# Optimization experiments

Measured on AMD Instinct MI355X. Metric: run time of the kernel, lower is better.

The kernel has to match this reference:

```python
import jax, jax.numpy as jnp
import numpy as np
from jax import lax

CLIP = 0.2
GAMMA = 1.0
LAM = 0.95
B, S = 256, 16384


def setup_inputs() -> dict:
    key = jax.random.key(0)
    k0, k1, k2, k3, k4, k5 = jax.random.split(key, 6)
    return {
        "rewards": jax.random.normal(k0, (B, S), jnp.float32),
        "values": jax.random.normal(k1, (B, S), jnp.float32),
        "new_log_probs": jax.random.normal(k2, (B, S), jnp.float32),
        "old_log_probs": jax.random.normal(k3, (B, S), jnp.float32),
        "new_values": jax.random.normal(k4, (B, S), jnp.float32),
        "act_masks": jax.random.randint(k5, (B, S), 0, 2, jnp.int32),
    }


def _mask_mean(loss, mask):
    # (loss * mask).sum(-1) / clamp(mask.sum(-1), 1e-8)
    return (loss * mask).sum(-1) / jnp.maximum(mask.sum(-1), 1e-8)


def _gae(rewards, values):
    # delta_t = r_t + gamma * V_{t+1} - V_t   (V_S := 0 bootstrap)
    next_values = jnp.concatenate([values[:, 1:], jnp.zeros_like(values[:, :1])], axis=1)
    deltas = rewards + GAMMA * next_values - values  # [B,S]
    decay = GAMMA * LAM

    def step(gae, delta):  # reverse-time linear recurrence
        gae = delta + decay * gae
        return gae, gae

    _, adv = lax.scan(step, jnp.zeros(deltas.shape[0], deltas.dtype), deltas.T, reverse=True)
    advantages = adv.T  # [B,S], in forward time order
    returns = advantages + values
    return advantages, returns


def reference(rewards, values, new_log_probs, old_log_probs, new_values, act_masks):
    mask = act_masks.astype(rewards.dtype)
    advantages, returns = _gae(rewards, values)

    # clipped PPO surrogate
    ratio = jnp.exp(new_log_probs - old_log_probs)
    surr1 = ratio * advantages
    surr2 = jnp.clip(ratio, 1.0 - CLIP, 1.0 + CLIP) * advantages
    p_loss = _mask_mean(-jnp.minimum(surr1, surr2), mask)  # [B]

    # masked value MSE against GAE returns
    v_loss = _mask_mean((new_values - returns) ** 2, mask)  # [B]

    return jnp.stack([p_loss, v_loss])  # [2, B]
```

## Files before the change

kernel.cpp:

```cpp
#include <hip/hip_runtime.h>

constexpr int B_DIM  = 256;
constexpr int S_DIM  = 16384;
constexpr int SEG    = 1024;
constexpr int NSEG   = S_DIM / SEG;
constexpr int HALO   = 256;
constexpr float DECAY   = 0.95f;
constexpr float CLIP_LO = 0.8f;
constexpr float CLIP_HI = 1.2f;

__host__ __device__ constexpr float fpow(float x, int n) {
    float r = 1.0f;
    for (int i = 0; i < n; ++i) r *= x;
    return r;
}

__device__ __forceinline__ float dpow4(int e) {
    float p = 1.0f;
    if (e & 1)  p *= fpow(DECAY, 4);
    if (e & 2)  p *= fpow(DECAY, 8);
    if (e & 4)  p *= fpow(DECAY, 16);
    if (e & 8)  p *= fpow(DECAY, 32);
    if (e & 16) p *= fpow(DECAY, 64);
    if (e & 32) p *= fpow(DECAY, 128);
    return p;
}

__global__ __launch_bounds__(256) void ppo_seg(
    const float* __restrict__ rewards,
    const float* __restrict__ values,
    const float* __restrict__ nlp,
    const float* __restrict__ olp,
    const float* __restrict__ nval,
    const int*   __restrict__ amask,
    double* __restrict__ part)
{
    const int l   = threadIdx.x & 63;
    const int wid = (blockIdx.x << 2) | (threadIdx.x >> 6);
    const int row = wid >> 4;
    const int seg = wid & 15;
    const size_t base = (size_t)row * S_DIM + (size_t)seg * SEG;
    const size_t i4   = base + 4 * (size_t)l;

    float4 r4[4], v4[4];
    #pragma unroll
    for (int q = 0; q < 4; ++q) {
        r4[q] = *reinterpret_cast<const float4*>(rewards + i4 + 256 * q);
        v4[q] = *reinterpret_cast<const float4*>(values  + i4 + 256 * q);
    }

    float G = 0.0f;
    float v_end = 0.0f;
    if (seg < NSEG - 1) {
        float4 rh = *reinterpret_cast<const float4*>(rewards + i4 + SEG);
        float4 vh = *reinterpret_cast<const float4*>(values  + i4 + SEG);
        float vhe = values[base + SEG + HALO];
        float vn = __shfl(vh.x, (l + 1) & 63);
        if (l == 63) vn = vhe;
        const float d0 = rh.x + vh.y - vh.x;
        const float d1 = rh.y + vh.z - vh.y;
        const float d2 = rh.z + vh.w - vh.z;
        const float d3 = rh.w + vn   - vh.w;
        const float c  = fmaf(DECAY, fmaf(DECAY, fmaf(DECAY, d3, d2), d1), d0);
        float u = dpow4(l) * c;
        #pragma unroll
        for (int m = 1; m < 64; m <<= 1) u += __shfl_xor(u, m);
        G = u;
        v_end = __shfl(vh.x, 0);
    }

    const float h1 = __shfl(v4[1].x, 0);
    const float h2 = __shfl(v4[2].x, 0);
    const float h3 = __shfl(v4[3].x, 0);
    const float nx[4] = {h1, h2, h3, v_end};

    float d[16];
    #pragma unroll
    for (int q = 0; q < 4; ++q) {
        float vn = __shfl(v4[q].x, (l + 1) & 63);
        if (l == 63) vn = nx[q];
        d[4*q+0] = r4[q].x + v4[q].y - v4[q].x;
        d[4*q+1] = r4[q].y + v4[q].z - v4[q].y;
        d[4*q+2] = r4[q].z + v4[q].w - v4[q].z;
        d[4*q+3] = r4[q].w + vn      - v4[q].w;
    }

    float s[4];
    #pragma unroll
    for (int q = 0; q < 4; ++q)
        s[q] = fmaf(DECAY, fmaf(DECAY, fmaf(DECAY, d[4*q+3], d[4*q+2]), d[4*q+1]), d[4*q+0]);

    #pragma unroll
    for (int st = 1; st < 64; st <<= 1) {
        const float f = fpow(DECAY, 4 * st);
        #pragma unroll
        for (int q = 0; q < 4; ++q) {
            float o = __shfl(s[q], min(l + st, 63));
            s[q] = (l < 64 - st) ? fmaf(f, o, s[q]) : s[q];
        }
    }

    constexpr float A256 = fpow(DECAY, 256);
    const float W1 = __shfl(s[1], 0);
    const float W2 = __shfl(s[2], 0);
    const float W3 = __shfl(s[3], 0);
    const float g3 = G;
    const float g2 = fmaf(A256, g3, W3);
    const float g1 = fmaf(A256, g2, W2);
    const float g0 = fmaf(A256, g1, W1);
    const float gq[4] = {g0, g1, g2, g3};

    const float pw = dpow4(63 - l);
    #pragma unroll
    for (int q = 0; q < 4; ++q) {
        const float sn  = __shfl(s[q], (l + 1) & 63);
        const float gin = (l < 63) ? fmaf(pw, gq[q], sn) : gq[q];
        float g = gin;
        g = fmaf(DECAY, g, d[4*q+3]); d[4*q+3] = g;
        g = fmaf(DECAY, g, d[4*q+2]); d[4*q+2] = g;
        g = fmaf(DECAY, g, d[4*q+1]); d[4*q+1] = g;
        g = fmaf(DECAY, g, d[4*q+0]); d[4*q+0] = g;
    }

    double sp = 0.0, sv = 0.0;
    float  sm = 0.0f;
    #pragma unroll
    for (int q = 0; q < 4; ++q) {
        const float4 a = *reinterpret_cast<const float4*>(nlp   + i4 + 256 * q);
        const float4 o = *reinterpret_cast<const float4*>(olp   + i4 + 256 * q);
        const float4 n = *reinterpret_cast<const float4*>(nval  + i4 + 256 * q);
        const int4   m = *reinterpret_cast<const int4*>  (amask + i4 + 256 * q);
        const float av[4] = {a.x, a.y, a.z, a.w};
        const float ov[4] = {o.x, o.y, o.z, o.w};
        const float nv[4] = {n.x, n.y, n.z, n.w};
        const int   mv[4] = {m.x, m.y, m.z, m.w};
        const float vv[4] = {v4[q].x, v4[q].y, v4[q].z, v4[q].w};
        #pragma unroll
        for (int j = 0; j < 4; ++j) {
            const float adv   = d[4*q+j];
            const float ratio = __expf(av[j] - ov[j]);
            const float s1    = ratio * adv;
            const float s2    = fminf(fmaxf(ratio, CLIP_LO), CLIP_HI) * adv;
            const float pl    = -fminf(s1, s2);
            const float mm    = (float)mv[j];
            sp += (double)(pl * mm);
            const float vd = nv[j] - (adv + vv[j]);
            sv += (double)(vd * vd) * (double)mm;
            sm += mm;
        }
    }

    #pragma unroll
    for (int m = 1; m < 64; m <<= 1) {
        sp += __shfl_xor(sp, m);
        sv += __shfl_xor(sv, m);
        sm += __shfl_xor(sm, m);
    }
    if (l == 0) {
        double* p = part + (size_t)wid * 3;
        p[0] = sp; p[1] = sv; p[2] = (double)sm;
    }
}

__global__ __launch_bounds__(256) void ppo_final(
    const double* __restrict__ part, float* __restrict__ out)
{
    const int b = threadIdx.x;
    double P = 0.0, V = 0.0, M = 0.0;
    #pragma unroll
    for (int s2 = 0; s2 < NSEG; ++s2) {
        const double* p = part + ((size_t)b * NSEG + s2) * 3;
        P += p[0]; V += p[1]; M += p[2];
    }
    const double Md = fmax(M, 1e-8);
    out[b]         = (float)(P / Md);
    out[B_DIM + b] = (float)(V / Md);
}

extern "C" void kernel_launch(void* const* d_in, const int* in_sizes, int n_in,
                              void* d_out, int out_size, void* d_ws, size_t ws_size,
                              hipStream_t stream) {
    const float* rewards = (const float*)d_in[0];
    const float* values  = (const float*)d_in[1];
    const float* nlp     = (const float*)d_in[2];
    const float* olp     = (const float*)d_in[3];
    const float* nval    = (const float*)d_in[4];
    const int*   amask   = (const int*)  d_in[5];
    float* out = (float*)d_out;
    double* part = (double*)d_ws;

    ppo_seg<<<B_DIM * NSEG / 4, 256, 0, stream>>>(rewards, values, nlp, olp, nval, amask, part);
    ppo_final<<<1, 256, 0, stream>>>(part, out);
}
```

Before: 24.75 us.

## Fuse final row reduction via last-block atomic counter and prefetch log-prob loads

```diff
diff --git a/kernel.cpp b/kernel.cpp
--- a/kernel.cpp
+++ b/kernel.cpp
@@ -8,6 +8,9 @@
 constexpr float DECAY   = 0.95f;
 constexpr float CLIP_LO = 0.8f;
 constexpr float CLIP_HI = 1.2f;
+
+constexpr size_t PART_BYTES = (size_t)B_DIM * NSEG * 3 * sizeof(double);
+constexpr size_t CNT_OFF    = PART_BYTES;
 
 __host__ __device__ constexpr float fpow(float x, int n) {
     float r = 1.0f;
@@ -33,10 +36,13 @@
     const float* __restrict__ olp,
     const float* __restrict__ nval,
     const int*   __restrict__ amask,
-    double* __restrict__ part)
+    double* __restrict__ part,
+    unsigned int* __restrict__ cnt,
+    float* __restrict__ out)
 {
     const int l   = threadIdx.x & 63;
-    const int wid = (blockIdx.x << 2) | (threadIdx.x >> 6);
+    const int wv  = threadIdx.x >> 6;
+    const int wid = (blockIdx.x << 2) | wv;
     const int row = wid >> 4;
     const int seg = wid & 15;
     const size_t base = (size_t)row * S_DIM + (size_t)seg * SEG;
@@ -48,13 +54,23 @@
         r4[q] = *reinterpret_cast<const float4*>(rewards + i4 + 256 * q);
         v4[q] = *reinterpret_cast<const float4*>(values  + i4 + 256 * q);
     }
-
-    float G = 0.0f;
-    float v_end = 0.0f;
-    if (seg < NSEG - 1) {
-        float4 rh = *reinterpret_cast<const float4*>(rewards + i4 + SEG);
-        float4 vh = *reinterpret_cast<const float4*>(values  + i4 + SEG);
-        float vhe = values[base + SEG + HALO];
+    const bool has_halo = (seg < NSEG - 1);
+    float4 rh = {0,0,0,0}, vh = {0,0,0,0};
+    float vhe = 0.0f;
+    if (has_halo) {
+        rh  = *reinterpret_cast<const float4*>(rewards + i4 + SEG);
+        vh  = *reinterpret_cast<const float4*>(values  + i4 + SEG);
+        vhe = values[base + SEG + HALO];
+    }
+    float4 a4[4], o4[4];
+    #pragma unroll
+    for (int q = 0; q < 4; ++q) {
+        a4[q] = *reinterpret_cast<const float4*>(nlp + i4 + 256 * q);
+        o4[q] = *reinterpret_cast<const float4*>(olp + i4 + 256 * q);
+    }
+
+    float G = 0.0f, v_end = 0.0f;
+    if (has_halo) {
         float vn = __shfl(vh.x, (l + 1) & 63);
         if (l == 63) vn = vhe;
         const float d0 = rh.x + vh.y - vh.x;
@@ -126,12 +142,10 @@
     float  sm = 0.0f;
     #pragma unroll
     for (int q = 0; q < 4; ++q) {
-        const float4 a = *reinterpret_cast<const float4*>(nlp   + i4 + 256 * q);
-        const float4 o = *reinterpret_cast<const float4*>(olp   + i4 + 256 * q);
         const float4 n = *reinterpret_cast<const float4*>(nval  + i4 + 256 * q);
         const int4   m = *reinterpret_cast<const int4*>  (amask + i4 + 256 * q);
-        const float av[4] = {a.x, a.y, a.z, a.w};
-        const float ov[4] = {o.x, o.y, o.z, o.w};
+        const float av[4] = {a4[q].x, a4[q].y, a4[q].z, a4[q].w};
+        const float ov[4] = {o4[q].x, o4[q].y, o4[q].z, o4[q].w};
         const float nv[4] = {n.x, n.y, n.z, n.w};
         const int   mv[4] = {m.x, m.y, m.z, m.w};
         const float vv[4] = {v4[q].x, v4[q].y, v4[q].z, v4[q].w};
@@ -160,21 +174,34 @@
         double* p = part + (size_t)wid * 3;
         p[0] = sp; p[1] = sv; p[2] = (double)sm;
     }
-}
-
-__global__ __launch_bounds__(256) void ppo_final(
-    const double* __restrict__ part, float* __restrict__ out)
-{
-    const int b = threadIdx.x;
-    double P = 0.0, V = 0.0, M = 0.0;
-    #pragma unroll
-    for (int s2 = 0; s2 < NSEG; ++s2) {
-        const double* p = part + ((size_t)b * NSEG + s2) * 3;
-        P += p[0]; V += p[1]; M += p[2];
-    }
-    const double Md = fmax(M, 1e-8);
-    out[b]         = (float)(P / Md);
-    out[B_DIM + b] = (float)(V / Md);
+
+    __shared__ unsigned int lastFlag;
+    __syncthreads();
+    if (threadIdx.x == 0) {
+        __threadfence();
+        const unsigned int old = atomicAdd(&cnt[row], 1u);
+        lastFlag = (old == 3u) ? 1u : 0u;
+    }
+    __syncthreads();
+    if (lastFlag && wv == 0) {
+        __threadfence();
+        double P = 0.0, V = 0.0, M = 0.0;
+        if (l < NSEG) {
+            const double* p = part + ((size_t)row * NSEG + l) * 3;
+            P = p[0]; V = p[1]; M = p[2];
+        }
+        #pragma unroll
+        for (int m = 1; m < NSEG; m <<= 1) {
+            P += __shfl_xor(P, m);
+            V += __shfl_xor(V, m);
+            M += __shfl_xor(M, m);
+        }
+        if (l == 0) {
+            const double Md = fmax(M, 1e-8);
+            out[row]         = (float)(P / Md);
+            out[B_DIM + row] = (float)(V / Md);
+        }
+    }
 }
 
 extern "C" void kernel_launch(void* const* d_in, const int* in_sizes, int n_in,
@@ -187,8 +214,12 @@
     const float* nval    = (const float*)d_in[4];
     const int*   amask   = (const int*)  d_in[5];
     float* out = (float*)d_out;
-    double* part = (double*)d_ws;
-
-    ppo_seg<<<B_DIM * NSEG / 4, 256, 0, stream>>>(rewards, values, nlp, olp, nval, amask, part);
-    ppo_final<<<1, 256, 0, stream>>>(part, out);
-}
+
+    double*       part = (double*)d_ws;
+    unsigned int* cnt  = (unsigned int*)((char*)d_ws + CNT_OFF);
+
+    hipMemsetAsync(cnt, 0, B_DIM * sizeof(unsigned int), stream);
+
+    ppo_seg<<<B_DIM * NSEG / 4, 256, 0, stream>>>(
+        rewards, values, nlp, olp, nval, amask, part, cnt, out);
+}
```

After: 66.77 us. 170% more time.

## Halve segment size and share boundary carries between waves via LDS

Applied to the files above, without the earlier changes.

```diff
diff --git a/kernel.cpp b/kernel.cpp
--- a/kernel.cpp
+++ b/kernel.cpp
@@ -1,10 +1,11 @@
 #include <hip/hip_runtime.h>
 
-constexpr int B_DIM  = 256;
-constexpr int S_DIM  = 16384;
-constexpr int SEG    = 1024;
-constexpr int NSEG   = S_DIM / SEG;
-constexpr int HALO   = 256;
+constexpr int B_DIM = 256;
+constexpr int S_DIM = 16384;
+constexpr int SEG   = 512;
+constexpr int NSEG  = S_DIM / SEG;
+constexpr int HALO  = 128;
+constexpr int NSEG_TOT = B_DIM * NSEG;
 constexpr float DECAY   = 0.95f;
 constexpr float CLIP_LO = 0.8f;
 constexpr float CLIP_HI = 1.2f;
@@ -15,6 +16,16 @@
     return r;
 }
 
+__device__ __forceinline__ float dpow2(int e) {
+    float p = 1.0f;
+    if (e & 1)  p *= fpow(DECAY, 2);
+    if (e & 2)  p *= fpow(DECAY, 4);
+    if (e & 4)  p *= fpow(DECAY, 8);
+    if (e & 8)  p *= fpow(DECAY, 16);
+    if (e & 16) p *= fpow(DECAY, 32);
+    if (e & 32) p *= fpow(DECAY, 64);
+    return p;
+}
 __device__ __forceinline__ float dpow4(int e) {
     float p = 1.0f;
     if (e & 1)  p *= fpow(DECAY, 4);
@@ -33,86 +44,100 @@
     const float* __restrict__ olp,
     const float* __restrict__ nval,
     const int*   __restrict__ amask,
-    double* __restrict__ part)
+    double* __restrict__ pP,
+    double* __restrict__ pV,
+    double* __restrict__ pM)
 {
     const int l   = threadIdx.x & 63;
-    const int wid = (blockIdx.x << 2) | (threadIdx.x >> 6);
-    const int row = wid >> 4;
-    const int seg = wid & 15;
+    const int wv  = threadIdx.x >> 6;
+    const int wid = (blockIdx.x << 2) | wv;
+    const int row = wid >> 5;
+    const int seg = wid & 31;
     const size_t base = (size_t)row * S_DIM + (size_t)seg * SEG;
     const size_t i4   = base + 4 * (size_t)l;
 
-    float4 r4[4], v4[4];
-    #pragma unroll
-    for (int q = 0; q < 4; ++q) {
+    float4 r4[2], v4[2];
+    #pragma unroll
+    for (int q = 0; q < 2; ++q) {
         r4[q] = *reinterpret_cast<const float4*>(rewards + i4 + 256 * q);
         v4[q] = *reinterpret_cast<const float4*>(values  + i4 + 256 * q);
     }
 
-    float G = 0.0f;
-    float v_end = 0.0f;
-    if (seg < NSEG - 1) {
-        float4 rh = *reinterpret_cast<const float4*>(rewards + i4 + SEG);
-        float4 vh = *reinterpret_cast<const float4*>(values  + i4 + SEG);
-        float vhe = values[base + SEG + HALO];
-        float vn = __shfl(vh.x, (l + 1) & 63);
-        if (l == 63) vn = vhe;
-        const float d0 = rh.x + vh.y - vh.x;
-        const float d1 = rh.y + vh.z - vh.y;
-        const float d2 = rh.z + vh.w - vh.z;
-        const float d3 = rh.w + vn   - vh.w;
-        const float c  = fmaf(DECAY, fmaf(DECAY, fmaf(DECAY, d3, d2), d1), d0);
-        float u = dpow4(l) * c;
-        #pragma unroll
-        for (int m = 1; m < 64; m <<= 1) u += __shfl_xor(u, m);
-        G = u;
-        v_end = __shfl(vh.x, 0);
-    }
+    const bool isw3     = (wv == 3);
+    const bool has_next = (seg < NSEG - 1);
+    float2 rh = {0, 0}, vh = {0, 0};
+    float  vhe = 0.0f;
+    if (isw3 && has_next) {
+        rh  = *reinterpret_cast<const float2*>(rewards + base + SEG + 2 * l);
+        vh  = *reinterpret_cast<const float2*>(values  + base + SEG + 2 * l);
+        vhe = values[base + SEG + HALO];
+    }
+
+    __shared__ float segV[4];
+    __shared__ float segT[4];
+    if (l == 0) segV[wv] = v4[0].x;
+    __syncthreads();
+
+    float v_end;
+    if (!isw3)          v_end = segV[wv + 1];
+    else if (has_next)  v_end = __shfl(vh.x, 0);
+    else                v_end = 0.0f;
 
     const float h1 = __shfl(v4[1].x, 0);
-    const float h2 = __shfl(v4[2].x, 0);
-    const float h3 = __shfl(v4[3].x, 0);
-    const float nx[4] = {h1, h2, h3, v_end};
-
-    float d[16];
-    #pragma unroll
-    for (int q = 0; q < 4; ++q) {
+    const float nx2[2] = {h1, v_end};
+    float d[8];
+    #pragma unroll
+    for (int q = 0; q < 2; ++q) {
         float vn = __shfl(v4[q].x, (l + 1) & 63);
-        if (l == 63) vn = nx[q];
+        if (l == 63) vn = nx2[q];
         d[4*q+0] = r4[q].x + v4[q].y - v4[q].x;
         d[4*q+1] = r4[q].y + v4[q].z - v4[q].y;
         d[4*q+2] = r4[q].z + v4[q].w - v4[q].z;
         d[4*q+3] = r4[q].w + vn      - v4[q].w;
     }
 
-    float s[4];
-    #pragma unroll
-    for (int q = 0; q < 4; ++q)
+    float s[2];
+    #pragma unroll
+    for (int q = 0; q < 2; ++q)
         s[q] = fmaf(DECAY, fmaf(DECAY, fmaf(DECAY, d[4*q+3], d[4*q+2]), d[4*q+1]), d[4*q+0]);
 
     #pragma unroll
     for (int st = 1; st < 64; st <<= 1) {
         const float f = fpow(DECAY, 4 * st);
         #pragma unroll
-        for (int q = 0; q < 4; ++q) {
+        for (int q = 0; q < 2; ++q) {
             float o = __shfl(s[q], min(l + st, 63));
             s[q] = (l < 64 - st) ? fmaf(f, o, s[q]) : s[q];
         }
     }
 
     constexpr float A256 = fpow(DECAY, 256);
+    const float W0 = __shfl(s[0], 0);
     const float W1 = __shfl(s[1], 0);
-    const float W2 = __shfl(s[2], 0);
-    const float W3 = __shfl(s[3], 0);
-    const float g3 = G;
-    const float g2 = fmaf(A256, g3, W3);
-    const float g1 = fmaf(A256, g2, W2);
+
+    float Gh = 0.0f;
+    if (isw3 && has_next) {
+        float vn = __shfl(vh.x, (l + 1) & 63);
+        if (l == 63) vn = vhe;
+        const float hd0 = rh.x + vh.y - vh.x;
+        const float hd1 = rh.y + vn   - vh.y;
+        const float c   = fmaf(DECAY, hd1, hd0);
+        float u = dpow2(l) * c;
+        #pragma unroll
+        for (int m = 1; m < 64; m <<= 1) u += __shfl_xor(u, m);
+        Gh = u;
+    }
+
+    if (l == 0) segT[wv] = fmaf(A256, W1, W0);
+    __syncthreads();
+    const float G  = (!isw3) ? segT[wv + 1] : Gh;
+    const float g1 = G;
     const float g0 = fmaf(A256, g1, W1);
-    const float gq[4] = {g0, g1, g2, g3};
+    const float gq[2] = {g0, g1};
 
     const float pw = dpow4(63 - l);
     #pragma unroll
-    for (int q = 0; q < 4; ++q) {
+    for (int q = 0; q < 2; ++q) {
         const float sn  = __shfl(s[q], (l + 1) & 63);
         const float gin = (l < 63) ? fmaf(pw, gq[q], sn) : gq[q];
         float g = gin;
@@ -125,7 +150,7 @@
     double sp = 0.0, sv = 0.0;
     float  sm = 0.0f;
     #pragma unroll
-    for (int q = 0; q < 4; ++q) {
+    for (int q = 0; q < 2; ++q) {
         const float4 a = *reinterpret_cast<const float4*>(nlp   + i4 + 256 * q);
         const float4 o = *reinterpret_cast<const float4*>(olp   + i4 + 256 * q);
         const float4 n = *reinterpret_cast<const float4*>(nval  + i4 + 256 * q);
@@ -156,25 +181,32 @@
         sv += __shfl_xor(sv, m);
         sm += __shfl_xor(sm, m);
     }
-    if (l == 0) {
-        double* p = part + (size_t)wid * 3;
-        p[0] = sp; p[1] = sv; p[2] = (double)sm;
-    }
+    if (l == 0) { pP[wid] = sp; pV[wid] = sv; pM[wid] = (double)sm; }
 }
 
 __global__ __launch_bounds__(256) void ppo_final(
-    const double* __restrict__ part, float* __restrict__ out)
+    const double* __restrict__ pP,
+    const double* __restrict__ pV,
+    const double* __restrict__ pM,
+    float* __restrict__ out)
 {
-    const int b = threadIdx.x;
-    double P = 0.0, V = 0.0, M = 0.0;
-    #pragma unroll
-    for (int s2 = 0; s2 < NSEG; ++s2) {
-        const double* p = part + ((size_t)b * NSEG + s2) * 3;
-        P += p[0]; V += p[1]; M += p[2];
-    }
-    const double Md = fmax(M, 1e-8);
-    out[b]         = (float)(P / Md);
-    out[B_DIM + b] = (float)(V / Md);
+    const int t   = threadIdx.x;
+    const int g   = t >> 5;
+    const int ln  = t & 31;
+    const int row = (blockIdx.x << 3) | g;
+    const int idx = (row << 5) | ln;
+    double P = pP[idx], V = pV[idx], M = pM[idx];
+    #pragma unroll
+    for (int m = 1; m < 32; m <<= 1) {
+        P += __shfl_xor(P, m);
+        V += __shfl_xor(V, m);
+        M += __shfl_xor(M, m);
+    }
+    if (ln == 0) {
+        const double Md = fmax(M, 1e-8);
+        out[row]         = (float)(P / Md);
+        out[B_DIM + row] = (float)(V / Md);
+    }
 }
 
 extern "C" void kernel_launch(void* const* d_in, const int* in_sizes, int n_in,
@@ -187,8 +219,12 @@
     const float* nval    = (const float*)d_in[4];
     const int*   amask   = (const int*)  d_in[5];
     float* out = (float*)d_out;
-    double* part = (double*)d_ws;
-
-    ppo_seg<<<B_DIM * NSEG / 4, 256, 0, stream>>>(rewards, values, nlp, olp, nval, amask, part);
-    ppo_final<<<1, 256, 0, stream>>>(part, out);
-}
+
+    double* pP = (double*)d_ws;
+    double* pV = pP + NSEG_TOT;
+    double* pM = pV + NSEG_TOT;
+
+    ppo_seg<<<NSEG_TOT / 4, 256, 0, stream>>>(
+        rewards, values, nlp, olp, nval, amask, pP, pV, pM);
+    ppo_final<<<32, 256, 0, stream>>>(pP, pV, pM, out);
+}
```

New measurement: 23.89 us. 3.5% less time.

## Fuse row into one 1024-thread block with shared-memory segment carry and reduction

Applied to the files above, without the earlier changes.

```diff
diff --git a/kernel.cpp b/kernel.cpp
--- a/kernel.cpp
+++ b/kernel.cpp
@@ -1,13 +1,16 @@
 #include <hip/hip_runtime.h>
 
-constexpr int B_DIM  = 256;
-constexpr int S_DIM  = 16384;
-constexpr int SEG    = 1024;
-constexpr int NSEG   = S_DIM / SEG;
-constexpr int HALO   = 256;
+constexpr int B_DIM    = 256;
+constexpr int S_DIM    = 16384;
+constexpr int NTHREADS = 1024;
+constexpr int NWAVES   = 16;
+constexpr int SEG      = 1024;
 constexpr float DECAY   = 0.95f;
 constexpr float CLIP_LO = 0.8f;
 constexpr float CLIP_HI = 1.2f;
+
+using f32x4 = __attribute__((ext_vector_type(4))) float;
+using i32x4 = __attribute__((ext_vector_type(4))) int;
 
 __host__ __device__ constexpr float fpow(float x, int n) {
     float r = 1.0f;
@@ -26,48 +29,30 @@
     return p;
 }
 
-__global__ __launch_bounds__(256) void ppo_seg(
+__global__ __launch_bounds__(NTHREADS) void ppo_row(
     const float* __restrict__ rewards,
     const float* __restrict__ values,
     const float* __restrict__ nlp,
     const float* __restrict__ olp,
     const float* __restrict__ nval,
     const int*   __restrict__ amask,
-    double* __restrict__ part)
+    float* __restrict__ out)
 {
     const int l   = threadIdx.x & 63;
-    const int wid = (blockIdx.x << 2) | (threadIdx.x >> 6);
-    const int row = wid >> 4;
-    const int seg = wid & 15;
-    const size_t base = (size_t)row * S_DIM + (size_t)seg * SEG;
+    const int wv  = threadIdx.x >> 6;
+    const int row = blockIdx.x;
+    const size_t base = (size_t)row * S_DIM + (size_t)wv * SEG;
     const size_t i4   = base + 4 * (size_t)l;
 
-    float4 r4[4], v4[4];
+    f32x4 r4[4], v4[4];
     #pragma unroll
     for (int q = 0; q < 4; ++q) {
-        r4[q] = *reinterpret_cast<const float4*>(rewards + i4 + 256 * q);
-        v4[q] = *reinterpret_cast<const float4*>(values  + i4 + 256 * q);
+        r4[q] = __builtin_nontemporal_load(reinterpret_cast<const f32x4*>(rewards + i4 + 256 * q));
+        v4[q] = __builtin_nontemporal_load(reinterpret_cast<const f32x4*>(values  + i4 + 256 * q));
     }
 
-    float G = 0.0f;
     float v_end = 0.0f;
-    if (seg < NSEG - 1) {
-        float4 rh = *reinterpret_cast<const float4*>(rewards + i4 + SEG);
-        float4 vh = *reinterpret_cast<const float4*>(values  + i4 + SEG);
-        float vhe = values[base + SEG + HALO];
-        float vn = __shfl(vh.x, (l + 1) & 63);
-        if (l == 63) vn = vhe;
-        const float d0 = rh.x + vh.y - vh.x;
-        const float d1 = rh.y + vh.z - vh.y;
-        const float d2 = rh.z + vh.w - vh.z;
-        const float d3 = rh.w + vn   - vh.w;
-        const float c  = fmaf(DECAY, fmaf(DECAY, fmaf(DECAY, d3, d2), d1), d0);
-        float u = dpow4(l) * c;
-        #pragma unroll
-        for (int m = 1; m < 64; m <<= 1) u += __shfl_xor(u, m);
-        G = u;
-        v_end = __shfl(vh.x, 0);
-    }
+    if (wv < NWAVES - 1) v_end = values[base + SEG];
 
     const float h1 = __shfl(v4[1].x, 0);
     const float h2 = __shfl(v4[2].x, 0);
@@ -101,9 +86,21 @@
     }
 
     constexpr float A256 = fpow(DECAY, 256);
+    const float W0 = __shfl(s[0], 0);
     const float W1 = __shfl(s[1], 0);
     const float W2 = __shfl(s[2], 0);
     const float W3 = __shfl(s[3], 0);
+    const float T  = fmaf(A256, fmaf(A256, fmaf(A256, W3, W2), W1), W0);
+
+    __shared__ float segT[NWAVES];
+    if (l == 0) segT[wv] = T;
+    __syncthreads();
+
+    constexpr float A1024 = fpow(DECAY, 1024);
+    float G = 0.0f;
+    for (int w = NWAVES - 1; w > wv; --w)
+        G = fmaf(A1024, G, segT[w]);
+
     const float g3 = G;
     const float g2 = fmaf(A256, g3, W3);
     const float g1 = fmaf(A256, g2, W2);
@@ -122,14 +119,13 @@
         g = fmaf(DECAY, g, d[4*q+0]); d[4*q+0] = g;
     }
 
-    double sp = 0.0, sv = 0.0;
-    float  sm = 0.0f;
+    float sp = 0.0f, sv = 0.0f, sm = 0.0f;
     #pragma unroll
     for (int q = 0; q < 4; ++q) {
-        const float4 a = *reinterpret_cast<const float4*>(nlp   + i4 + 256 * q);
-        const float4 o = *reinterpret_cast<const float4*>(olp   + i4 + 256 * q);
-        const float4 n = *reinterpret_cast<const float4*>(nval  + i4 + 256 * q);
-        const int4   m = *reinterpret_cast<const int4*>  (amask + i4 + 256 * q);
+        const f32x4 a = __builtin_nontemporal_load(reinterpret_cast<const f32x4*>(nlp   + i4 + 256 * q));
+        const f32x4 o = __builtin_nontemporal_load(reinterpret_cast<const f32x4*>(olp   + i4 + 256 * q));
+        const f32x4 n = __builtin_nontemporal_load(reinterpret_cast<const f32x4*>(nval  + i4 + 256 * q));
+        const i32x4 m = __builtin_nontemporal_load(reinterpret_cast<const i32x4*>(amask + i4 + 256 * q));
         const float av[4] = {a.x, a.y, a.z, a.w};
         const float ov[4] = {o.x, o.y, o.z, o.w};
         const float nv[4] = {n.x, n.y, n.z, n.w};
@@ -143,9 +139,9 @@
             const float s2    = fminf(fmaxf(ratio, CLIP_LO), CLIP_HI) * adv;
             const float pl    = -fminf(s1, s2);
             const float mm    = (float)mv[j];
-            sp += (double)(pl * mm);
+            sp = fmaf(pl, mm, sp);
             const float vd = nv[j] - (adv + vv[j]);
-            sv += (double)(vd * vd) * (double)mm;
+            sv = fmaf(vd * vd, mm, sv);
             sm += mm;
         }
     }
@@ -156,25 +152,28 @@
         sv += __shfl_xor(sv, m);
         sm += __shfl_xor(sm, m);
     }
-    if (l == 0) {
-        double* p = part + (size_t)wid * 3;
-        p[0] = sp; p[1] = sv; p[2] = (double)sm;
+    __shared__ double redP[NWAVES];
+    __shared__ double redV[NWAVES];
+    __shared__ float  redM[NWAVES];
+    if (l == 0) { redP[wv] = (double)sp; redV[wv] = (double)sv; redM[wv] = sm; }
+    __syncthreads();
+
+    if (threadIdx.x < NWAVES) {
+        double P = redP[threadIdx.x];
+        double V = redV[threadIdx.x];
+        float  M = redM[threadIdx.x];
+        #pragma unroll
+        for (int m = 1; m < NWAVES; m <<= 1) {
+            P += __shfl_xor(P, m);
+            V += __shfl_xor(V, m);
+            M += __shfl_xor(M, m);
+        }
+        if (threadIdx.x == 0) {
+            const double Md = fmax((double)M, 1e-8);
+            out[row]         = (float)(P / Md);
+            out[B_DIM + row] = (float)(V / Md);
+        }
     }
-}
-
-__global__ __launch_bounds__(256) void ppo_final(
-    const double* __restrict__ part, float* __restrict__ out)
-{
-    const int b = threadIdx.x;
-    double P = 0.0, V = 0.0, M = 0.0;
-    #pragma unroll
-    for (int s2 = 0; s2 < NSEG; ++s2) {
-        const double* p = part + ((size_t)b * NSEG + s2) * 3;
-        P += p[0]; V += p[1]; M += p[2];
-    }
-    const double Md = fmax(M, 1e-8);
-    out[b]         = (float)(P / Md);
-    out[B_DIM + b] = (float)(V / Md);
 }
 
 extern "C" void kernel_launch(void* const* d_in, const int* in_sizes, int n_in,
@@ -187,8 +186,7 @@
     const float* nval    = (const float*)d_in[4];
     const int*   amask   = (const int*)  d_in[5];
     float* out = (float*)d_out;
-    double* part = (double*)d_ws;
 
-    ppo_seg<<<B_DIM * NSEG / 4, 256, 0, stream>>>(rewards, values, nlp, olp, nval, amask, part);
-    ppo_final<<<1, 256, 0, stream>>>(part, out);
+    ppo_row<<<B_DIM, NTHREADS, 0, stream>>>(
+        rewards, values, nlp, olp, nval, amask, out);
 }
```

After: 25.36 us. 1.02x slower.
